# Kernel optimization log

Measured on AMD Instinct MI355X. Metric: run time of the kernel, lower is better.

Reference implementation:

```python
import itertools
import jax, jax.numpy as jnp
import numpy as np

FS = 16000
MAX_TAU = 40
C_SOUND = 343.0
MIC_DISTANCE_FROM_WALL = 0.5
MIN_SPEAKER_HEIGHT = 1.0
MAX_SPEAKER_HEIGHT = 2.0
ROOM = (6.0, 5.0, 3.0)
DENSITY = (0.1, 0.1, 0.1)
N_MICS = 8


def _build_geometry():
    # 8-mic circular array, radius 0.4 m, centered in the room
    ang = np.arange(N_MICS) * 2.0 * np.pi / N_MICS
    receivers = np.stack([3.0 + 0.4 * np.cos(ang),
                          2.5 + 0.4 * np.sin(ang),
                          1.5 * np.ones(N_MICS)], axis=1).astype(np.float32)  # [M,3]
    combinations = np.array(list(itertools.combinations(range(N_MICS), 2)), dtype=np.int32)  # [P,2]
    # candidate grid (same nesting order as the original list comprehension)
    xs = np.arange(MIC_DISTANCE_FROM_WALL, ROOM[0] + DENSITY[0], DENSITY[0], dtype=np.float32)
    ys = np.arange(0.0, ROOM[1] + DENSITY[1], DENSITY[1], dtype=np.float32)
    zs = np.arange(MIN_SPEAKER_HEIGHT, MAX_SPEAKER_HEIGHT + DENSITY[2], DENSITY[2], dtype=np.float32)
    grid_x = np.stack(np.meshgrid(xs, ys, zs, indexing='ij'), axis=-1).reshape(-1, 3)  # [G,3]
    # true TDOA per grid point / pair -> delay index into GCC output of length 2*MAX_TAU+1
    rp = receivers[combinations]                                   # [P,2,3]
    d = np.linalg.norm(grid_x[:, None, None, :] - rp[None], axis=-1)  # [G,P,2]
    tdoa = (d[..., 0] - d[..., 1]) / C_SOUND * FS                  # samples
    tau = np.clip(MAX_TAU + np.round(tdoa), 0, 2 * MAX_TAU).astype(np.int32)  # [G,P]
    rec_centroid = receivers.mean(axis=0)                          # [3]
    return grid_x, tau, combinations, rec_centroid


def setup_inputs() -> dict:
    key = jax.random.key(0)
    signal = jax.random.normal(key, (16, N_MICS, 4096), dtype=jnp.float32)
    grid_x, tau, combinations, rec_centroid = _build_geometry()
    return {
        "signal": signal,
        "grid_x": jnp.asarray(grid_x),
        "tau": jnp.asarray(tau),
        "combinations": jnp.asarray(combinations),
        "rec_centroid": jnp.asarray(rec_centroid),
    }


def reference(signal, grid_x, tau, combinations, rec_centroid):
    B, M, N = signal.shape
    P = combinations.shape[0]
    # GCC-PHAT per mic pair
    pairs = signal[:, combinations, :]                    # [B,P,2,N]
    S = jnp.fft.rfft(pairs, axis=-1)                      # [B,P,2,F]
    X = S[..., 0, :] * jnp.conj(S[..., 1, :])             # cross-spectrum [B,P,F]
    phat = X / (jnp.abs(X) + 1e-12)
    cc = jnp.fft.irfft(phat, n=N, axis=-1)                # [B,P,N]
    # lags -MAX_TAU..MAX_TAU -> length 2*MAX_TAU+1
    cc = jnp.concatenate([cc[..., -MAX_TAU:], cc[..., :MAX_TAU + 1]], axis=-1)  # [B,P,2T+1]
    # gather per grid point / pair (avoids materializing [B,G,P,2T+1])
    gathered = cc[:, jnp.arange(P)[None, :], tau]         # [B,G,P]
    power = gathered.sum(axis=-1)                         # SRP map [B,G]
    idx = jnp.argmax(power, axis=-1)                      # [B]
    x = grid_x[idx]                                       # [B,3]
    return x - rec_centroid
```

## Files before the change

kernel.cpp:

```cpp
#include <hip/hip_runtime.h>

#define N_FFT 4096
#define NH    2048
#define NBINS 2049
#define NLAGS 81
#define MAXTAU 40
#define NSEG  8
#define SEGLEN 256
#define PI_F 3.14159265358979323846f
#define PAD(i) ((i) + ((i) >> 4))

__global__ __launch_bounds__(1024)
void rfft_kernel(const float* __restrict__ sig,
                 float* __restrict__ S,
                 float* __restrict__ cc, int ccN) {
    int bm  = (int)blockIdx.x;
    int tid = (int)threadIdx.x;

    __shared__ float2 data[PAD(NH - 1) + 1];
    __shared__ float2 tw[NH / 2];

    for (int i = bm * 1024 + tid; i < ccN; i += (int)gridDim.x * 1024)
        cc[i] = 0.0f;

    {
        float sv, cv;
        sincosf(-(2.0f * PI_F / (float)NH) * (float)tid, &sv, &cv);
        tw[tid] = make_float2(cv, sv);
    }

    const float2* sp = (const float2*)(sig + (size_t)bm * N_FFT);
    for (int i = tid; i < NH; i += 1024) {
        float2 v = sp[i];
        int j = (int)(__brev((unsigned)i) >> 21);
        data[PAD(j)] = v;
    }
    __syncthreads();

    for (int s = 1; s <= 11; ++s) {
        int half = 1 << (s - 1);
        int g  = tid >> (s - 1);
        int j  = tid & (half - 1);
        int i0 = (g << s) + j;
        int i1 = i0 + half;
        float2 w = tw[j << (11 - s)];
        float2 u = data[PAD(i0)];
        float2 v = data[PAD(i1)];
        float vr = v.x * w.x - v.y * w.y;
        float vi = v.x * w.y + v.y * w.x;
        data[PAD(i0)] = make_float2(u.x + vr, u.y + vi);
        data[PAD(i1)] = make_float2(u.x - vr, u.y - vi);
        __syncthreads();
    }

    float* So = S + (size_t)bm * NBINS * 2;
    for (int k = tid; k < NBINS; k += 1024) {
        float2 Zk = data[PAD(k & (NH - 1))];
        float2 Zm = data[PAD((NH - k) & (NH - 1))];
        float er = 0.5f * (Zk.x + Zm.x);
        float ei = 0.5f * (Zk.y - Zm.y);
        float dr = Zk.x - Zm.x;
        float di = Zk.y + Zm.y;
        float orr = 0.5f * di;
        float oii = -0.5f * dr;
        float sv, cv;
        sincosf(-(2.0f * PI_F / (float)N_FFT) * (float)k, &sv, &cv);
        So[k * 2]     = er + cv * orr - sv * oii;
        So[k * 2 + 1] = ei + cv * oii + sv * orr;
    }
}

#define NCH 6
#define CHLEN 43
__global__ __launch_bounds__(256)
void phat_cc_kernel(const float* __restrict__ S,
                    const int* __restrict__ comb,
                    float* __restrict__ cc, int P) {
    int id  = (int)blockIdx.x;
    int seg = id & (NSEG - 1);
    int bp  = id >> 3;
    int b   = bp / P;
    int p   = bp % P;
    int ma = comb[p * 2 + 0];
    int mb = comb[p * 2 + 1];
    const float2* Sa = (const float2*)(S + ((size_t)(b * 8 + ma)) * NBINS * 2);
    const float2* Sb = (const float2*)(S + ((size_t)(b * 8 + mb)) * NBINS * 2);

    int k0 = seg * SEGLEN;
    int k1 = (seg == NSEG - 1) ? NBINS : (k0 + SEGLEN);

    __shared__ float2 phs[SEGLEN + 1];
    __shared__ float partCr[41 * NCH];
    __shared__ float partCi[41 * NCH];

    int tid = (int)threadIdx.x;
    for (int k = k0 + tid; k < k1; k += 256) {
        float2 a = Sa[k];
        float2 c = Sb[k];
        float Xr = a.x * c.x + a.y * c.y;
        float Xi = a.y * c.x - a.x * c.y;
        float mag = sqrtf(Xr * Xr + Xi * Xi);
        float w = (k == 0 || k == 2048) ? 1.0f : 2.0f;
        float inv = w / (mag + 1e-12f);
        phs[k - k0] = make_float2(Xr * inv, Xi * inv);
    }
    __syncthreads();

    if (tid < 41 * NCH) {
        int n = tid % 41;
        int c = tid / 41;
        int kk0 = k0 + c * CHLEN;
        int kk1 = kk0 + CHLEN;
        if (kk1 > k1) kk1 = k1;

        float step = (2.0f * PI_F / (float)N_FFT) * (float)n;
        float sv, cv;
        sincosf(step, &sv, &cv);
        float wr = cv, wi = sv;
        sincosf(step * (float)kk0, &sv, &cv);
        float rr = cv, ri = sv;

        float Cr = 0.0f, Ci = 0.0f;
        for (int k = kk0; k < kk1; ++k) {
            float2 ph = phs[k - k0];
            Cr = fmaf(ph.x, rr, Cr);
            Ci = fmaf(ph.y, ri, Ci);
            float nr = rr * wr - ri * wi;
            float ni = rr * wi + ri * wr;
            rr = nr; ri = ni;
        }
        partCr[tid] = Cr;
        partCi[tid] = Ci;
    }
    __syncthreads();

    if (tid < 41) {
        float Cr = 0.0f, Ci = 0.0f;
        #pragma unroll
        for (int c = 0; c < NCH; ++c) {
            Cr += partCr[tid + 41 * c];
            Ci += partCi[tid + 41 * c];
        }
        float* outp = cc + (size_t)bp * NLAGS;
        atomicAdd(&outp[MAXTAU + tid], Cr - Ci);
        if (tid > 0) atomicAdd(&outp[MAXTAU - tid], Cr + Ci);
    }
}

__global__ __launch_bounds__(256)
void power_argmax_kernel(const float* __restrict__ cc,
                         const int* __restrict__ tau,
                         int G, int P,
                         float* __restrict__ pval,
                         int* __restrict__ pidx, int nchunks) {
    int b     = (int)blockIdx.y;
    int chunk = (int)blockIdx.x;
    int tid   = (int)threadIdx.x;

    __shared__ float ccs[28 * NLAGS];
    const float* csrc = cc + (size_t)b * P * NLAGS;
    for (int i = tid; i < 28 * NLAGS; i += 256)
        ccs[i] = csrc[i] * (1.0f / (float)N_FFT);
    __syncthreads();

    int g = chunk * 256 + tid;
    float v = -1e30f;
    int   gi = 0x7fffffff;
    if (g < G) {
        const int4* tp = (const int4*)(tau + (size_t)g * 28);
        v = 0.0f;
        #pragma unroll
        for (int q = 0; q < 7; ++q) {
            int4 tv = tp[q];
            v += ccs[(q * 4 + 0) * NLAGS + tv.x];
            v += ccs[(q * 4 + 1) * NLAGS + tv.y];
            v += ccs[(q * 4 + 2) * NLAGS + tv.z];
            v += ccs[(q * 4 + 3) * NLAGS + tv.w];
        }
        gi = g;
    }

    #pragma unroll
    for (int off = 32; off > 0; off >>= 1) {
        float v2 = __shfl_down(v, off);
        int   i2 = __shfl_down(gi, off);
        if (v2 > v || (v2 == v && i2 < gi)) { v = v2; gi = i2; }
    }
    __shared__ float wval[4];
    __shared__ int   widx[4];
    int lane = tid & 63, wv = tid >> 6;
    if (lane == 0) { wval[wv] = v; widx[wv] = gi; }
    __syncthreads();
    if (tid == 0) {
        #pragma unroll
        for (int w = 1; w < 4; ++w) {
            float v2 = wval[w]; int i2 = widx[w];
            if (v2 > v || (v2 == v && i2 < gi)) { v = v2; gi = i2; }
        }
        pval[b * nchunks + chunk] = v;
        pidx[b * nchunks + chunk] = gi;
    }
}

__global__ void finalize_kernel(const float* __restrict__ pval,
                                const int* __restrict__ pidx, int nchunks,
                                const float* __restrict__ grid_x,
                                const float* __restrict__ rec_centroid,
                                float* __restrict__ out) {
    int b = (int)blockIdx.x;
    int l = (int)threadIdx.x;
    float v = -1e30f; int gi = 0x7fffffff;
    for (int j = l; j < nchunks; j += 64) {
        float v2 = pval[b * nchunks + j];
        int   i2 = pidx[b * nchunks + j];
        if (v2 > v || (v2 == v && i2 < gi)) { v = v2; gi = i2; }
    }
    #pragma unroll
    for (int off = 32; off > 0; off >>= 1) {
        float v2 = __shfl_down(v, off);
        int   i2 = __shfl_down(gi, off);
        if (v2 > v || (v2 == v && i2 < gi)) { v = v2; gi = i2; }
    }
    if (l == 0) {
        for (int c = 0; c < 3; ++c)
            out[b * 3 + c] = grid_x[(size_t)gi * 3 + c] - rec_centroid[c];
    }
}

extern "C" void kernel_launch(void* const* d_in, const int* in_sizes, int n_in,
                              void* d_out, int out_size, void* d_ws, size_t ws_size,
                              hipStream_t stream) {
    const float* signal       = (const float*)d_in[0];
    const float* grid_x       = (const float*)d_in[1];
    const int*   tau          = (const int*)d_in[2];
    const int*   comb         = (const int*)d_in[3];
    const float* rec_centroid = (const float*)d_in[4];
    float* out = (float*)d_out;

    int G  = in_sizes[1] / 3;
    int P  = in_sizes[3] / 2;
    int BM = in_sizes[0] / N_FFT;
    int B  = BM / 8;
    int BP = B * P;

    float* S  = (float*)d_ws;
    float* cc = S + (size_t)BM * NBINS * 2;
    int nchunks = (G + 255) / 256;
    float* pval = cc + (size_t)BP * NLAGS;
    int*   pidx = (int*)(pval + (size_t)B * nchunks);

    rfft_kernel<<<BM, 1024, 0, stream>>>(signal, S, cc, BP * NLAGS);
    phat_cc_kernel<<<BP * NSEG, 256, 0, stream>>>(S, comb, cc, P);
    power_argmax_kernel<<<dim3(nchunks, B), 256, 0, stream>>>(cc, tau, G, P, pval, pidx, nchunks);
    finalize_kernel<<<B, 64, 0, stream>>>(pval, pidx, nchunks, grid_x, rec_centroid, out);
}
```

Baseline: 97.38 us.

## Use radix-4 FFT stages with 512 threads and reuse twiddle table for post-processing

Replaces the 11 radix-2 butterfly stages with five fused radix-4 stages plus one final radix-2 stage, running on 512 threads per block. This halves the number of barriers and shared-memory round trips. The real-FFT post-processing step now derives its twiddles from the shared table plus a fixed rotation instead of calling sincosf per bin. This lowers transcendental cost but adds slight rounding differences in the twiddles and halves the thread count per block.

```diff
diff --git a/kernel.cpp b/kernel.cpp
--- a/kernel.cpp
+++ b/kernel.cpp
@@ -10,7 +10,14 @@
 #define PI_F 3.14159265358979323846f
 #define PAD(i) ((i) + ((i) >> 4))
 
-__global__ __launch_bounds__(1024)
+#define CQ 0.99999882345f
+#define SQ 0.00153398019f
+
+__device__ __forceinline__ float2 cmul(float2 a, float2 b) {
+    return make_float2(a.x * b.x - a.y * b.y, a.x * b.y + a.y * b.x);
+}
+
+__global__ __launch_bounds__(512)
 void rfft_kernel(const float* __restrict__ sig,
                  float* __restrict__ S,
                  float* __restrict__ cc, int ccN) {
@@ -20,41 +27,65 @@
     __shared__ float2 data[PAD(NH - 1) + 1];
     __shared__ float2 tw[NH / 2];
 
-    for (int i = bm * 1024 + tid; i < ccN; i += (int)gridDim.x * 1024)
+    for (int i = bm * 512 + tid; i < ccN; i += (int)gridDim.x * 512)
         cc[i] = 0.0f;
 
-    {
+    for (int j = tid; j < NH / 2; j += 512) {
         float sv, cv;
-        sincosf(-(2.0f * PI_F / (float)NH) * (float)tid, &sv, &cv);
-        tw[tid] = make_float2(cv, sv);
+        sincosf(-(2.0f * PI_F / (float)NH) * (float)j, &sv, &cv);
+        tw[j] = make_float2(cv, sv);
     }
 
     const float2* sp = (const float2*)(sig + (size_t)bm * N_FFT);
-    for (int i = tid; i < NH; i += 1024) {
+    for (int i = tid; i < NH; i += 512) {
         float2 v = sp[i];
         int j = (int)(__brev((unsigned)i) >> 21);
         data[PAD(j)] = v;
     }
     __syncthreads();
 
-    for (int s = 1; s <= 11; ++s) {
-        int half = 1 << (s - 1);
+    for (int s = 1; s <= 9; s += 2) {
+        int h  = 1 << (s - 1);
+        int j  = tid & (h - 1);
         int g  = tid >> (s - 1);
-        int j  = tid & (half - 1);
-        int i0 = (g << s) + j;
-        int i1 = i0 + half;
-        float2 w = tw[j << (11 - s)];
+        int i0 = (g << (s + 1)) + j;
+        int i1 = i0 + h, i2 = i0 + 2 * h, i3 = i0 + 3 * h;
+
+        float2 w1 = tw[j << (11 - s)];
+        float2 wA = tw[j << (10 - s)];
+        float2 wB = tw[(j + h) << (10 - s)];
+
+        float2 a = data[PAD(i0)];
+        float2 b = data[PAD(i1)];
+        float2 c = data[PAD(i2)];
+        float2 d = data[PAD(i3)];
+
+        float2 wb = cmul(w1, b), wd = cmul(w1, d);
+        float2 a1 = make_float2(a.x + wb.x, a.y + wb.y);
+        float2 b1 = make_float2(a.x - wb.x, a.y - wb.y);
+        float2 c1 = make_float2(c.x + wd.x, c.y + wd.y);
+        float2 d1 = make_float2(c.x - wd.x, c.y - wd.y);
+        float2 wc = cmul(wA, c1), wdd = cmul(wB, d1);
+        data[PAD(i0)] = make_float2(a1.x + wc.x,  a1.y + wc.y);
+        data[PAD(i2)] = make_float2(a1.x - wc.x,  a1.y - wc.y);
+        data[PAD(i1)] = make_float2(b1.x + wdd.x, b1.y + wdd.y);
+        data[PAD(i3)] = make_float2(b1.x - wdd.x, b1.y - wdd.y);
+        __syncthreads();
+    }
+
+    for (int t = tid; t < 1024; t += 512) {
+        int i0 = t, i1 = t + 1024;
+        float2 w = tw[t];
         float2 u = data[PAD(i0)];
         float2 v = data[PAD(i1)];
-        float vr = v.x * w.x - v.y * w.y;
-        float vi = v.x * w.y + v.y * w.x;
-        data[PAD(i0)] = make_float2(u.x + vr, u.y + vi);
-        data[PAD(i1)] = make_float2(u.x - vr, u.y - vi);
-        __syncthreads();
-    }
+        float2 wv = cmul(w, v);
+        data[PAD(i0)] = make_float2(u.x + wv.x, u.y + wv.y);
+        data[PAD(i1)] = make_float2(u.x - wv.x, u.y - wv.y);
+    }
+    __syncthreads();
 
     float* So = S + (size_t)bm * NBINS * 2;
-    for (int k = tid; k < NBINS; k += 1024) {
+    for (int k = tid; k < NBINS; k += 512) {
         float2 Zk = data[PAD(k & (NH - 1))];
         float2 Zm = data[PAD((NH - k) & (NH - 1))];
         float er = 0.5f * (Zk.x + Zm.x);
@@ -63,10 +94,17 @@
         float di = Zk.y + Zm.y;
         float orr = 0.5f * di;
         float oii = -0.5f * dr;
-        float sv, cv;
-        sincosf(-(2.0f * PI_F / (float)N_FFT) * (float)k, &sv, &cv);
-        So[k * 2]     = er + cv * orr - sv * oii;
-        So[k * 2 + 1] = ei + cv * oii + sv * orr;
+        float2 W;
+        if (k == 2048) {
+            W = make_float2(-1.0f, 0.0f);
+        } else {
+            float2 t = tw[k >> 1];
+            if (k & 1) W = make_float2(t.x * CQ + t.y * SQ,
+                                       t.y * CQ - t.x * SQ);
+            else       W = t;
+        }
+        So[k * 2]     = er + W.x * orr - W.y * oii;
+        So[k * 2 + 1] = ei + W.x * oii + W.y * orr;
     }
 }
 
@@ -249,7 +287,7 @@
     float* pval = cc + (size_t)BP * NLAGS;
     int*   pidx = (int*)(pval + (size_t)B * nchunks);
 
-    rfft_kernel<<<BM, 1024, 0, stream>>>(signal, S, cc, BP * NLAGS);
+    rfft_kernel<<<BM, 512, 0, stream>>>(signal, S, cc, BP * NLAGS);
     phat_cc_kernel<<<BP * NSEG, 256, 0, stream>>>(S, comb, cc, P);
     power_argmax_kernel<<<dim3(nchunks, B), 256, 0, stream>>>(cc, tau, G, P, pval, pidx, nchunks);
     finalize_kernel<<<B, 64, 0, stream>>>(pval, pidx, nchunks, grid_x, rec_centroid, out);
```

New measurement: 96.62 us. No clear change (-0.8%).
